# Optimization experiments

Hardware: AMD Instinct MI355X
Metric: run time of the kernel (lower is better)

Reference implementation:

```python
import jax, jax.numpy as jnp
import numpy as np

N = 1024          # sentence length
VW, DW = 100000, 300   # word vocab / embed dim
VP, DP = 64, 100       # pos vocab / embed dim
DV = DW + DP           # len_data_vec = 400 (LSTM in & hidden size)
H = 512                # MLP hidden
F = 128                # feature vec


def _lstm_dir(xs, h0, c0, Wih, Whh, bih, bhh):
    # PyTorch LSTM cell: gates ordered i, f, g, o
    def step(carry, x):
        h, c = carry
        g = x @ Wih.T + bih + h @ Whh.T + bhh
        i, f, gg, o = jnp.split(g, 4)
        i = jax.nn.sigmoid(i)
        f = jax.nn.sigmoid(f)
        gg = jnp.tanh(gg)
        o = jax.nn.sigmoid(o)
        c = f * c + i * gg
        h = o * jnp.tanh(c)
        return (h, c), h
    _, hs = jax.lax.scan(step, (h0, c0), xs)
    return hs  # [n, DV]


def setup_inputs() -> dict:
    key = jax.random.key(0)
    ks = jax.random.split(key, 24)
    s = 0.05
    inp = {
        'word_ids': jax.random.randint(ks[0], (N,), 0, VW),
        'pos_ids': jax.random.randint(ks[1], (N,), 0, VP),
        'h0': jax.random.normal(ks[2], (2, DV), jnp.float32),
        'c0': jax.random.normal(ks[3], (2, DV), jnp.float32),
        'word_emb': jax.random.normal(ks[4], (VW, DW), jnp.float32) * s,
        'pos_emb': jax.random.normal(ks[5], (VP, DP), jnp.float32) * s,
        'Wih_f': jax.random.normal(ks[6], (4 * DV, DV), jnp.float32) * s,
        'Whh_f': jax.random.normal(ks[7], (4 * DV, DV), jnp.float32) * s,
        'bih_f': jax.random.normal(ks[8], (4 * DV,), jnp.float32) * s,
        'bhh_f': jax.random.normal(ks[9], (4 * DV,), jnp.float32) * s,
        'Wih_b': jax.random.normal(ks[10], (4 * DV, DV), jnp.float32) * s,
        'Whh_b': jax.random.normal(ks[11], (4 * DV, DV), jnp.float32) * s,
        'bih_b': jax.random.normal(ks[12], (4 * DV,), jnp.float32) * s,
        'bhh_b': jax.random.normal(ks[13], (4 * DV,), jnp.float32) * s,
        'Wh1': jax.random.normal(ks[14], (H, 2 * DV), jnp.float32) * s,
        'bh1': jax.random.normal(ks[15], (H,), jnp.float32) * s,
        'Wh2': jax.random.normal(ks[16], (F, H), jnp.float32) * s,
        'bh2': jax.random.normal(ks[17], (F,), jnp.float32) * s,
        'Wd1': jax.random.normal(ks[18], (H, 2 * DV), jnp.float32) * s,
        'bd1': jax.random.normal(ks[19], (H,), jnp.float32) * s,
        'Wd2': jax.random.normal(ks[20], (F, H), jnp.float32) * s,
        'bd2': jax.random.normal(ks[21], (F,), jnp.float32) * s,
        'U_1': jax.random.normal(ks[22], (F, F), jnp.float32),
        'u_2': jax.random.normal(ks[23], (1, F), jnp.float32),
    }
    return inp


def reference(word_ids, pos_ids, h0, c0, word_emb, pos_emb,
              Wih_f, Whh_f, bih_f, bhh_f, Wih_b, Whh_b, bih_b, bhh_b,
              Wh1, bh1, Wh2, bh2, Wd1, bd1, Wd2, bd2, U_1, u_2):
    # Embedding gather + concat: x[i] = [word_emb; pos_emb]
    x = jnp.concatenate([word_emb[word_ids], pos_emb[pos_ids]], axis=-1)  # [n, DV]
    # BiLSTM (batch=1): forward dir and reversed dir, concat features
    r_f = _lstm_dir(x, h0[0], c0[0], Wih_f, Whh_f, bih_f, bhh_f)
    r_b = _lstm_dir(x[::-1], h0[1], c0[1], Wih_b, Whh_b, bih_b, bhh_b)[::-1]
    r = jnp.concatenate([r_f, r_b], axis=-1)  # [n, 2*DV]
    sr = jax.nn.sigmoid(r)
    # MLP_head / MLP_dep (clamp(min=0) == relu), batched over all tokens
    Hh = jax.nn.relu(sr @ Wh1.T + bh1) @ Wh2.T + bh2  # [n, F]
    Hd = jax.nn.relu(sr @ Wd1.T + bd1) @ Wd2.T + bd2  # [n, F]
    # Biaffine: adj[i,j] = h_i U h_j^T + h_i u_2^T
    adj = Hh @ U_1 @ Hd.T + Hh @ u_2.T  # [n, n] + [n, 1] broadcast
    return adj
```

## Files before the change

kernel.cpp:

```cpp
#include <hip/hip_runtime.h>
#include <math.h>

#define N_TOK 1024
#define DV    400
#define G4    1600
#define DWD   300
#define DPD   100
#define HID   512
#define FD    128
#define GWG   50
#define EPW   8
#define NCHK  (DV/4)

typedef unsigned uint32x4 __attribute__((ext_vector_type(4)));

__device__ __forceinline__ float sigmoidf_(float x){ return 1.0f/(1.0f+__expf(-x)); }
__device__ __forceinline__ float tanh_safe(float x){
    float t = __expf(-2.0f*fabsf(x));
    float r = (1.0f - t)/(1.0f + t);
    return copysignf(r, x);
}

#define LDA4(p) __hip_atomic_load((p), __ATOMIC_RELAXED, __HIP_MEMORY_SCOPE_AGENT)

#define PLD(X, P) asm volatile("global_load_dwordx4 %0, %1, off sc0 sc1" \
                               : "+&v"(X) : "v"(P) : "memory")
#define PWT(X)    asm volatile("s_waitcnt vmcnt(2)" : "+v"(X) :: "memory")

__global__ void k_gather(const int* __restrict__ wid, const int* __restrict__ pid,
                         const float* __restrict__ wemb, const float* __restrict__ pemb,
                         float* __restrict__ x)
{
    int t = blockIdx.x;
    int w = wid[t], p = pid[t];
    for (int k = threadIdx.x; k < DV; k += blockDim.x){
        float v = (k < DWD) ? wemb[(long)w*DWD + k] : pemb[p*DPD + (k - DWD)];
        x[t*DV + k] = v;
    }
}

__global__ void k_transpose(const float* __restrict__ U, float* __restrict__ Ut, int n)
{
    int j = blockIdx.y*16 + threadIdx.y;
    int k = blockIdx.x*16 + threadIdx.x;
    if (j < n && k < n) Ut[j*n + k] = U[k*n + j];
}

__global__ __launch_bounds__(256) void k_gemm_nt(
    const float* __restrict__ A, const float* __restrict__ B,
    const float* __restrict__ bias1, const float* __restrict__ rowbias,
    float* __restrict__ C, int M, int Nn, int K)
{
    const int BM = 64, BN = 64, BK = 16;
    __shared__ float As[BK][BM];
    __shared__ float Bs[BK][BN];
    int tid = threadIdx.x;
    int tx = tid & 15, ty = tid >> 4;
    int m0 = blockIdx.y*BM, n0 = blockIdx.x*BN;
    int lrow = tid >> 2, lk = (tid & 3) * 4;
    float acc[4][4] = {{0.f}};
    for (int k0 = 0; k0 < K; k0 += BK){
        const float4 av = *(const float4*)&A[(long)(m0+lrow)*K + k0 + lk];
        const float4 bv = *(const float4*)&B[(long)(n0+lrow)*K + k0 + lk];
        As[lk+0][lrow]=av.x; As[lk+1][lrow]=av.y; As[lk+2][lrow]=av.z; As[lk+3][lrow]=av.w;
        Bs[lk+0][lrow]=bv.x; Bs[lk+1][lrow]=bv.y; Bs[lk+2][lrow]=bv.z; Bs[lk+3][lrow]=bv.w;
        __syncthreads();
        #pragma unroll
        for (int kk = 0; kk < BK; ++kk){
            const float4 a = *(const float4*)&As[kk][ty*4];
            const float4 b = *(const float4*)&Bs[kk][tx*4];
            const float ar[4]={a.x,a.y,a.z,a.w}, br[4]={b.x,b.y,b.z,b.w};
            #pragma unroll
            for (int i=0;i<4;++i)
                #pragma unroll
                for (int j=0;j<4;++j) acc[i][j] += ar[i]*br[j];
        }
        __syncthreads();
    }
    #pragma unroll
    for (int i=0;i<4;++i){
        int m = m0 + ty*4 + i;
        float rb = rowbias ? rowbias[m] : 0.0f;
        #pragma unroll
        for (int j=0;j<4;++j){
            int n = n0 + tx*4 + j;
            float v = acc[i][j] + rb;
            if (bias1) v += bias1[n];
            C[(long)m*Nn + n] = v;
        }
    }
}

__global__ __launch_bounds__(256) void k_gemm_ntz(
    const float* __restrict__ A0, const float* __restrict__ A1,
    const float* __restrict__ B0, const float* __restrict__ B1,
    const float* __restrict__ c10, const float* __restrict__ c11,
    const float* __restrict__ c20, const float* __restrict__ c21,
    float* __restrict__ C0, float* __restrict__ C1,
    int M, int Nn, int K, int rev1, int relu)
{
    const float* A = blockIdx.z ? A1 : A0;
    const float* B = blockIdx.z ? B1 : B0;
    const float* bias1 = blockIdx.z ? c11 : c10;
    const float* bias2 = blockIdx.z ? c21 : c20;
    float* C = blockIdx.z ? C1 : C0;
    int revA = blockIdx.z ? rev1 : 0;

    const int BM = 64, BN = 64, BK = 16;
    __shared__ float As[BK][BM];
    __shared__ float Bs[BK][BN];
    int tid = threadIdx.x;
    int tx = tid & 15, ty = tid >> 4;
    int m0 = blockIdx.y*BM, n0 = blockIdx.x*BN;
    int lrow = tid >> 2, lk = (tid & 3) * 4;
    float acc[4][4] = {{0.f}};
    for (int k0 = 0; k0 < K; k0 += BK){
        int am = m0 + lrow; if (revA) am = M - 1 - am;
        const float4 av = *(const float4*)&A[(long)am*K + k0 + lk];
        const float4 bv = *(const float4*)&B[(long)(n0+lrow)*K + k0 + lk];
        As[lk+0][lrow]=av.x; As[lk+1][lrow]=av.y; As[lk+2][lrow]=av.z; As[lk+3][lrow]=av.w;
        Bs[lk+0][lrow]=bv.x; Bs[lk+1][lrow]=bv.y; Bs[lk+2][lrow]=bv.z; Bs[lk+3][lrow]=bv.w;
        __syncthreads();
        #pragma unroll
        for (int kk = 0; kk < BK; ++kk){
            const float4 a = *(const float4*)&As[kk][ty*4];
            const float4 b = *(const float4*)&Bs[kk][tx*4];
            const float ar[4]={a.x,a.y,a.z,a.w}, br[4]={b.x,b.y,b.z,b.w};
            #pragma unroll
            for (int i=0;i<4;++i)
                #pragma unroll
                for (int j=0;j<4;++j) acc[i][j] += ar[i]*br[j];
        }
        __syncthreads();
    }
    #pragma unroll
    for (int i=0;i<4;++i){
        int m = m0 + ty*4 + i;
        #pragma unroll
        for (int j=0;j<4;++j){
            int n = n0 + tx*4 + j;
            float v = acc[i][j];
            if (bias1) v += bias1[n];
            if (bias2) v += bias2[n];
            if (relu)  v = fmaxf(v, 0.0f);
            C[(long)m*Nn + n] = v;
        }
    }
}

__global__ __launch_bounds__(256) void k_lstm(
    const float* __restrict__ Whh_f, const float* __restrict__ Whh_b,
    const float* __restrict__ Xf, const float* __restrict__ Xb,
    const float* __restrict__ h0, const float* __restrict__ c0,
    unsigned* __restrict__ mbox)
{
    __shared__ float W_s[32][DV];
    __shared__ __align__(16) float hA[DV];
    __shared__ __align__(16) float hB[DV];

    int tid = threadIdx.x;
    int dir = blockIdx.x / GWG;
    int g   = blockIdx.x % GWG;
    int j0  = g * EPW;
    const float* Whh = dir ? Whh_b : Whh_f;
    const float* XX  = dir ? Xb    : Xf;
    unsigned* mb = mbox + (size_t)dir * N_TOK * DV;

    for (int idx = tid; idx < 32*DV; idx += 256){
        int rr = idx / DV, k = idx % DV;
        int grow_ = (rr >> 3) * DV + j0 + (rr & 7);
        W_s[rr][k] = Whh[(long)grow_*DV + k];
    }
    for (int idx = tid; idx < DV; idx += 256) hA[idx] = h0[dir*DV + idx];

    int w    = tid >> 6;
    int lane = tid & 63;
    int q    = lane >> 4;
    int eo   = (lane >> 3) & 1;
    int l    = lane & 7;
    int e    = 2*w + eo;
    int r    = q*8 + e;
    int grow = q*DV + j0 + e;
    bool owner = (q == 0) && (l == 0);
    float c_reg = owner ? c0[dir*DV + j0 + e] : 0.0f;

    int  cid   = tid;
    bool isPoll = (tid < NCHK) && (cid != 2*g) && (cid != 2*g + 1);
    __syncthreads();

    float xv_n = (l == 0) ? XX[grow] : 0.0f;

    bool dead = false;
    for (int t = 0; t < N_TOK; ++t){
        const float* hc = (t & 1) ? hB : hA;
        float*       hn = (t & 1) ? hA : hB;

        const unsigned* pc = mb + (size_t)t*DV + 4*cid;
        uint32x4 A = {0,0,0,0}, B = {0,0,0,0}, C = {0,0,0,0};
        if (isPoll){ PLD(A, pc); PLD(B, pc); PLD(C, pc); }

        float xv = xv_n;

        const float2* wrow = (const float2*)&W_s[r][0];
        const float2* hp   = (const float2*)hc;
        float sum = 0.0f;
        #pragma unroll
        for (int i = 0; i < 25; ++i){
            float2 wv = wrow[l + 8*i];
            float2 hv = hp[l + 8*i];
            sum = fmaf(wv.x, hv.x, sum);
            sum = fmaf(wv.y, hv.y, sum);
        }
        sum += __shfl_xor(sum, 1, 8);
        sum += __shfl_xor(sum, 2, 8);
        sum += __shfl_xor(sum, 4, 8);
        if (l == 0) sum += xv;

        float gi = __shfl(sum, eo*8 + 0,  64);
        float gf = __shfl(sum, eo*8 + 16, 64);
        float gg = __shfl(sum, eo*8 + 32, 64);
        float go = __shfl(sum, eo*8 + 48, 64);

        if (owner){
            float iv = sigmoidf_(gi), fv = sigmoidf_(gf);
            float gv = tanh_safe(gg), ov = sigmoidf_(go);
            c_reg = fv*c_reg + iv*gv;
            float hvv = ov * tanh_safe(c_reg);
            unsigned pk = __float_as_uint(hvv) | 1u;
            __hip_atomic_store(mb + (size_t)t*DV + j0 + e, pk,
                               __ATOMIC_RELAXED, __HIP_MEMORY_SCOPE_AGENT);
            hn[j0 + e] = hvv;
        }

        if (l == 0){
            int tn = (t + 1 < N_TOK) ? (t + 1) : t;
            xv_n = XX[(size_t)tn*G4 + grow];
        }

        if (isPoll && !dead){
            bool got = false;
            uint32x4 R;
            int fast = 0;
            while (fast < 64){
                PWT(A); if (A.x && A.y && A.z && A.w){ R = A; got = true; break; }
                PLD(A, pc);
                PWT(B); if (B.x && B.y && B.z && B.w){ R = B; got = true; break; }
                PLD(B, pc);
                PWT(C); if (C.x && C.y && C.z && C.w){ R = C; got = true; break; }
                PLD(C, pc);
                fast += 3;
            }
            if (got){
                float4 f;
                f.x = __uint_as_float(R.x); f.y = __uint_as_float(R.y);
                f.z = __uint_as_float(R.z); f.w = __uint_as_float(R.w);
                *(float4*)&hn[4*cid] = f;
            } else {
                bool d0=false,d1=false,d2=false,d3=false;
                int guard = 0;
                while (!(d0 && d1 && d2 && d3)){
                    if (!d0){ unsigned u = LDA4(pc+0); if (u){ hn[4*cid+0]=__uint_as_float(u); d0=true; } }
                    if (!d1){ unsigned u = LDA4(pc+1); if (u){ hn[4*cid+1]=__uint_as_float(u); d1=true; } }
                    if (!d2){ unsigned u = LDA4(pc+2); if (u){ hn[4*cid+2]=__uint_as_float(u); d2=true; } }
                    if (!d3){ unsigned u = LDA4(pc+3); if (u){ hn[4*cid+3]=__uint_as_float(u); d3=true; } }
                    if (++guard > (1 << 18)) { dead = true; break; }
                }
            }
        }
        __syncthreads();
    }
}

__global__ void k_sr(const float* __restrict__ mbox, float* __restrict__ sr)
{
    int t = blockIdx.x;
    const float* mF = mbox;
    const float* mB = mbox + (size_t)N_TOK * DV;
    for (int c = threadIdx.x; c < 2*DV; c += blockDim.x){
        float v = (c < DV) ? mF[(size_t)t*DV + c]
                           : mB[(size_t)(N_TOK-1-t)*DV + (c - DV)];
        sr[t*2*DV + c] = 1.0f/(1.0f+__expf(-v));
    }
}

__global__ void k_bvec(const float* __restrict__ Hh, const float* __restrict__ u2,
                       float* __restrict__ bvec)
{
    int i = blockIdx.x;
    int lane = threadIdx.x;
    float v = Hh[i*FD + lane]*u2[lane] + Hh[i*FD + 64 + lane]*u2[64 + lane];
    v += __shfl_xor(v, 1, 64);
    v += __shfl_xor(v, 2, 64);
    v += __shfl_xor(v, 4, 64);
    v += __shfl_xor(v, 8, 64);
    v += __shfl_xor(v, 16, 64);
    v += __shfl_xor(v, 32, 64);
    if (lane == 0) bvec[i] = v;
}

extern "C" void kernel_launch(void* const* d_in, const int* in_sizes, int n_in,
                              void* d_out, int out_size, void* d_ws, size_t ws_size,
                              hipStream_t stream)
{
    const int*   word_ids = (const int*)  d_in[0];
    const int*   pos_ids  = (const int*)  d_in[1];
    const float* h0    = (const float*)d_in[2];
    const float* c0    = (const float*)d_in[3];
    const float* wemb  = (const float*)d_in[4];
    const float* pemb  = (const float*)d_in[5];
    const float* Wih_f = (const float*)d_in[6];
    const float* Whh_f = (const float*)d_in[7];
    const float* bih_f = (const float*)d_in[8];
    const float* bhh_f = (const float*)d_in[9];
    const float* Wih_b = (const float*)d_in[10];
    const float* Whh_b = (const float*)d_in[11];
    const float* bih_b = (const float*)d_in[12];
    const float* bhh_b = (const float*)d_in[13];
    const float* Wh1   = (const float*)d_in[14];
    const float* bh1   = (const float*)d_in[15];
    const float* Wh2   = (const float*)d_in[16];
    const float* bh2   = (const float*)d_in[17];
    const float* Wd1   = (const float*)d_in[18];
    const float* bd1   = (const float*)d_in[19];
    const float* Wd2   = (const float*)d_in[20];
    const float* bd2   = (const float*)d_in[21];
    const float* U1    = (const float*)d_in[22];
    const float* u2    = (const float*)d_in[23];
    float* out = (float*)d_out;

    float* ws  = (float*)d_ws;
    float* x    = ws;
    float* Xf   = ws + 409600;
    float* Xb   = ws + 2048000;
    unsigned* mbox = (unsigned*)(ws + 3686400);
    float* sr   = ws + 4505600;
    float* T1h  = ws + 5324800;
    float* T1d  = ws + 5849088;
    float* Hh   = ws + 6373376;
    float* Hd   = ws + 6504448;
    float* G1   = ws + 6635520;
    float* Ut   = ws + 6766592;
    float* bvec = ws + 6782976;

    hipMemsetAsync(mbox, 0, (size_t)2*N_TOK*DV*sizeof(unsigned), stream);

    k_gather<<<N_TOK, 128, 0, stream>>>(word_ids, pos_ids, wemb, pemb, x);
    k_transpose<<<dim3(8,8), dim3(16,16), 0, stream>>>(U1, Ut, FD);

    dim3 blk(256);
    k_gemm_ntz<<<dim3(G4/64, N_TOK/64, 2), blk, 0, stream>>>(
        x, x, Wih_f, Wih_b, bih_f, bih_b, bhh_f, bhh_b, Xf, Xb,
        N_TOK, G4, DV, 1, 0);

    k_lstm<<<2*GWG, 256, 0, stream>>>(Whh_f, Whh_b, Xf, Xb, h0, c0, mbox);

    k_sr<<<N_TOK, 256, 0, stream>>>((const float*)mbox, sr);

    k_gemm_ntz<<<dim3(HID/64, N_TOK/64, 2), blk, 0, stream>>>(
        sr, sr, Wh1, Wd1, bh1, bd1, nullptr, nullptr, T1h, T1d,
        N_TOK, HID, 2*DV, 0, 1);
    k_gemm_ntz<<<dim3(FD/64, N_TOK/64, 2), blk, 0, stream>>>(
        T1h, T1d, Wh2, Wd2, bh2, bd2, nullptr, nullptr, Hh, Hd,
        N_TOK, FD, HID, 0, 0);
    k_bvec<<<N_TOK, 64, 0, stream>>>(Hh, u2, bvec);
    k_gemm_nt<<<dim3(FD/64,  N_TOK/64), blk, 0, stream>>>(Hh, Ut, nullptr, nullptr, G1,
                                                          N_TOK, FD, FD);
    k_gemm_nt<<<dim3(N_TOK/64, N_TOK/64), blk, 0, stream>>>(G1, Hd, nullptr, bvec, out,
                                                            N_TOK, N_TOK, FD);
}
```

Measured before the change: 2.926 ms.

## Pin each LSTM direction to one XCC and poll XCC-local L2 mailbox

Launches many blocks and keeps only those on XCC 0 and 1, assigning each direction's 50 workgroups through an atomic ticket so every block of a direction shares one L2. The h-exchange then writes a fast mailbox with sc0 stores and polls it with sc0 loads, which stay coherent within the XCC instead of going to device scope. A shadow copy is still written with agent-scope atomics and serves as a fallback after repeated fast-poll timeouts, and k_sr reads from it. The scheme assumes enough co-resident blocks land on each XCC, and it adds a second mailbox plus launch overhead for the blocks that exit immediately.

```diff
diff --git a/kernel.cpp b/kernel.cpp
--- a/kernel.cpp
+++ b/kernel.cpp
@@ -23,9 +23,9 @@
 
 #define LDA4(p) __hip_atomic_load((p), __ATOMIC_RELAXED, __HIP_MEMORY_SCOPE_AGENT)
 
-#define PLD(X, P) asm volatile("global_load_dwordx4 %0, %1, off sc0 sc1" \
-                               : "+&v"(X) : "v"(P) : "memory")
-#define PWT(X)    asm volatile("s_waitcnt vmcnt(2)" : "+v"(X) :: "memory")
+#define PLDF(X, P) asm volatile("global_load_dwordx4 %0, %1, off sc0" \
+                                : "+&v"(X) : "v"(P) : "memory")
+#define WT0(X)     asm volatile("s_waitcnt vmcnt(0)" : "+v"(X) :: "memory")
 
 __global__ void k_gather(const int* __restrict__ wid, const int* __restrict__ pid,
                          const float* __restrict__ wemb, const float* __restrict__ pemb,
@@ -152,19 +152,30 @@
     const float* __restrict__ Whh_f, const float* __restrict__ Whh_b,
     const float* __restrict__ Xf, const float* __restrict__ Xb,
     const float* __restrict__ h0, const float* __restrict__ c0,
-    unsigned* __restrict__ mbox)
+    unsigned* __restrict__ fastm, unsigned* __restrict__ shadow,
+    int* __restrict__ tickets)
 {
     __shared__ float W_s[32][DV];
     __shared__ __align__(16) float hA[DV];
     __shared__ __align__(16) float hB[DV];
+    __shared__ int rank_s;
+
+    unsigned xcc;
+    asm volatile("s_getreg_b32 %0, hwreg(HW_REG_XCC_ID)" : "=s"(xcc));
+    if (xcc > 1) return;
 
     int tid = threadIdx.x;
-    int dir = blockIdx.x / GWG;
-    int g   = blockIdx.x % GWG;
+    int dir = (int)xcc;
+    if (tid == 0) rank_s = atomicAdd(&tickets[dir], 1);
+    __syncthreads();
+    int g = rank_s;
+    if (g >= GWG) return;
+
     int j0  = g * EPW;
     const float* Whh = dir ? Whh_b : Whh_f;
     const float* XX  = dir ? Xb    : Xf;
-    unsigned* mb = mbox + (size_t)dir * N_TOK * DV;
+    unsigned* fm = fastm  + (size_t)dir * N_TOK * DV;
+    unsigned* sh = shadow + (size_t)dir * N_TOK * DV;
 
     for (int idx = tid; idx < 32*DV; idx += 256){
         int rr = idx / DV, k = idx % DV;
@@ -184,21 +195,17 @@
     bool owner = (q == 0) && (l == 0);
     float c_reg = owner ? c0[dir*DV + j0 + e] : 0.0f;
 
-    int  cid   = tid;
+    int  cid    = tid;
     bool isPoll = (tid < NCHK) && (cid != 2*g) && (cid != 2*g + 1);
     __syncthreads();
 
     float xv_n = (l == 0) ? XX[grow] : 0.0f;
 
-    bool dead = false;
+    bool dead = false, useFast = true;
+    int  fastFails = 0;
     for (int t = 0; t < N_TOK; ++t){
         const float* hc = (t & 1) ? hB : hA;
         float*       hn = (t & 1) ? hA : hB;
-
-        const unsigned* pc = mb + (size_t)t*DV + 4*cid;
-        uint32x4 A = {0,0,0,0}, B = {0,0,0,0}, C = {0,0,0,0};
-        if (isPoll){ PLD(A, pc); PLD(B, pc); PLD(C, pc); }
-
         float xv = xv_n;
 
         const float2* wrow = (const float2*)&W_s[r][0];
@@ -227,7 +234,10 @@
             c_reg = fv*c_reg + iv*gv;
             float hvv = ov * tanh_safe(c_reg);
             unsigned pk = __float_as_uint(hvv) | 1u;
-            __hip_atomic_store(mb + (size_t)t*DV + j0 + e, pk,
+            unsigned* fs = fm + (size_t)t*DV + j0 + e;
+            asm volatile("global_store_dword %0, %1, off sc0"
+                         :: "v"(fs), "v"(pk) : "memory");
+            __hip_atomic_store(sh + (size_t)t*DV + j0 + e, pk,
                                __ATOMIC_RELAXED, __HIP_MEMORY_SCOPE_AGENT);
             hn[j0 + e] = hvv;
         }
@@ -238,31 +248,36 @@
         }
 
         if (isPoll && !dead){
+            const unsigned* pf = fm + (size_t)t*DV + 4*cid;
+            const unsigned* ps = sh + (size_t)t*DV + 4*cid;
             bool got = false;
-            uint32x4 R;
-            int fast = 0;
-            while (fast < 64){
-                PWT(A); if (A.x && A.y && A.z && A.w){ R = A; got = true; break; }
-                PLD(A, pc);
-                PWT(B); if (B.x && B.y && B.z && B.w){ R = B; got = true; break; }
-                PLD(B, pc);
-                PWT(C); if (C.x && C.y && C.z && C.w){ R = C; got = true; break; }
-                PLD(C, pc);
-                fast += 3;
+            if (useFast){
+                uint32x4 A = {0,0,0,0};
+                PLDF(A, pf);
+                int it = 0;
+                for (;;){
+                    WT0(A);
+                    if (A.x && A.y && A.z && A.w){ got = true; break; }
+                    if (++it > 32) break;
+                    PLDF(A, pf);
+                }
+                if (got){
+                    float4 f;
+                    f.x = __uint_as_float(A.x); f.y = __uint_as_float(A.y);
+                    f.z = __uint_as_float(A.z); f.w = __uint_as_float(A.w);
+                    *(float4*)&hn[4*cid] = f;
+                } else {
+                    if (++fastFails >= 2) useFast = false;
+                }
             }
-            if (got){
-                float4 f;
-                f.x = __uint_as_float(R.x); f.y = __uint_as_float(R.y);
-                f.z = __uint_as_float(R.z); f.w = __uint_as_float(R.w);
-                *(float4*)&hn[4*cid] = f;
-            } else {
+            if (!got){
                 bool d0=false,d1=false,d2=false,d3=false;
                 int guard = 0;
                 while (!(d0 && d1 && d2 && d3)){
-                    if (!d0){ unsigned u = LDA4(pc+0); if (u){ hn[4*cid+0]=__uint_as_float(u); d0=true; } }
-                    if (!d1){ unsigned u = LDA4(pc+1); if (u){ hn[4*cid+1]=__uint_as_float(u); d1=true; } }
-                    if (!d2){ unsigned u = LDA4(pc+2); if (u){ hn[4*cid+2]=__uint_as_float(u); d2=true; } }
-                    if (!d3){ unsigned u = LDA4(pc+3); if (u){ hn[4*cid+3]=__uint_as_float(u); d3=true; } }
+                    if (!d0){ unsigned u = LDA4(ps+0); if (u){ hn[4*cid+0]=__uint_as_float(u); d0=true; } }
+                    if (!d1){ unsigned u = LDA4(ps+1); if (u){ hn[4*cid+1]=__uint_as_float(u); d1=true; } }
+                    if (!d2){ unsigned u = LDA4(ps+2); if (u){ hn[4*cid+2]=__uint_as_float(u); d2=true; } }
+                    if (!d3){ unsigned u = LDA4(ps+3); if (u){ hn[4*cid+3]=__uint_as_float(u); d3=true; } }
                     if (++guard > (1 << 18)) { dead = true; break; }
                 }
             }
@@ -271,11 +286,11 @@
     }
 }
 
-__global__ void k_sr(const float* __restrict__ mbox, float* __restrict__ sr)
+__global__ void k_sr(const float* __restrict__ shadow, float* __restrict__ sr)
 {
     int t = blockIdx.x;
-    const float* mF = mbox;
-    const float* mB = mbox + (size_t)N_TOK * DV;
+    const float* mF = shadow;
+    const float* mB = shadow + (size_t)N_TOK * DV;
     for (int c = threadIdx.x; c < 2*DV; c += blockDim.x){
         float v = (c < DV) ? mF[(size_t)t*DV + c]
                            : mB[(size_t)(N_TOK-1-t)*DV + (c - DV)];
@@ -332,17 +347,20 @@
     float* x    = ws;
     float* Xf   = ws + 409600;
     float* Xb   = ws + 2048000;
-    unsigned* mbox = (unsigned*)(ws + 3686400);
-    float* sr   = ws + 4505600;
-    float* T1h  = ws + 5324800;
-    float* T1d  = ws + 5849088;
-    float* Hh   = ws + 6373376;
-    float* Hd   = ws + 6504448;
-    float* G1   = ws + 6635520;
-    float* Ut   = ws + 6766592;
-    float* bvec = ws + 6782976;
-
-    hipMemsetAsync(mbox, 0, (size_t)2*N_TOK*DV*sizeof(unsigned), stream);
+    unsigned* fastm  = (unsigned*)(ws + 3686400);
+    unsigned* shadow = (unsigned*)(ws + 4505600);
+    float* sr   = ws + 5324800;
+    float* T1h  = ws + 6144000;
+    float* T1d  = ws + 6668288;
+    float* Hh   = ws + 7192576;
+    float* Hd   = ws + 7323648;
+    float* G1   = ws + 7454720;
+    float* Ut   = ws + 7585792;
+    float* bvec = ws + 7602176;
+    int*   tickets = (int*)(ws + 7603200);
+
+    hipMemsetAsync(fastm, 0, (size_t)2 * 2*N_TOK*DV*sizeof(unsigned), stream);
+    hipMemsetAsync(tickets, 0, 2*sizeof(int), stream);
 
     k_gather<<<N_TOK, 128, 0, stream>>>(word_ids, pos_ids, wemb, pemb, x);
     k_transpose<<<dim3(8,8), dim3(16,16), 0, stream>>>(U1, Ut, FD);
@@ -352,9 +370,10 @@
         x, x, Wih_f, Wih_b, bih_f, bih_b, bhh_f, bhh_b, Xf, Xb,
         N_TOK, G4, DV, 1, 0);
 
-    k_lstm<<<2*GWG, 256, 0, stream>>>(Whh_f, Whh_b, Xf, Xb, h0, c0, mbox);
-
-    k_sr<<<N_TOK, 256, 0, stream>>>((const float*)mbox, sr);
+    k_lstm<<<2048, 256, 0, stream>>>(Whh_f, Whh_b, Xf, Xb, h0, c0,
+                                     fastm, shadow, tickets);
+
+    k_sr<<<N_TOK, 256, 0, stream>>>((const float*)shadow, sr);
 
     k_gemm_ntz<<<dim3(HID/64, N_TOK/64, 2), blk, 0, stream>>>(
         sr, sr, Wh1, Wd1, bh1, bd1, nullptr, nullptr, T1h, T1d,
```

New measurement: 4.294 ms. 1.47x slower.

## Pad LSTM mailbox slots and poll per-element with scalar atomic loads

Applied to the files above, without the earlier changes.

The cross-block h-exchange mailbox is padded so each hidden element sits in its own 16-byte slot. Each thread now polls two scalar elements with a three-deep pipeline of relaxed atomic loads, replacing the earlier dwordx4 chunk polling done through inline asm. The next-step X prefetch is moved earlier, and workspace buffers are reshuffled so the larger mailbox fits. The aim is to avoid waiting on whole 4-element chunks and to reduce false sharing in the per-step handoff, at the cost of four times the mailbox memory and more load instructions per step.

```diff
diff --git a/kernel.cpp b/kernel.cpp
--- a/kernel.cpp
+++ b/kernel.cpp
@@ -10,9 +10,7 @@
 #define FD    128
 #define GWG   50
 #define EPW   8
-#define NCHK  (DV/4)
-
-typedef unsigned uint32x4 __attribute__((ext_vector_type(4)));
+#define PAD   4
 
 __device__ __forceinline__ float sigmoidf_(float x){ return 1.0f/(1.0f+__expf(-x)); }
 __device__ __forceinline__ float tanh_safe(float x){
@@ -21,11 +19,7 @@
     return copysignf(r, x);
 }
 
-#define LDA4(p) __hip_atomic_load((p), __ATOMIC_RELAXED, __HIP_MEMORY_SCOPE_AGENT)
-
-#define PLD(X, P) asm volatile("global_load_dwordx4 %0, %1, off sc0 sc1" \
-                               : "+&v"(X) : "v"(P) : "memory")
-#define PWT(X)    asm volatile("s_waitcnt vmcnt(2)" : "+v"(X) :: "memory")
+#define LDA(p) __hip_atomic_load((p), __ATOMIC_RELAXED, __HIP_MEMORY_SCOPE_AGENT)
 
 __global__ void k_gather(const int* __restrict__ wid, const int* __restrict__ pid,
                          const float* __restrict__ wemb, const float* __restrict__ pemb,
@@ -164,7 +158,7 @@
     int j0  = g * EPW;
     const float* Whh = dir ? Whh_b : Whh_f;
     const float* XX  = dir ? Xb    : Xf;
-    unsigned* mb = mbox + (size_t)dir * N_TOK * DV;
+    unsigned* mb = mbox + (size_t)dir * N_TOK * DV * PAD;
 
     for (int idx = tid; idx < 32*DV; idx += 256){
         int rr = idx / DV, k = idx % DV;
@@ -184,8 +178,9 @@
     bool owner = (q == 0) && (l == 0);
     float c_reg = owner ? c0[dir*DV + j0 + e] : 0.0f;
 
-    int  cid   = tid;
-    bool isPoll = (tid < NCHK) && (cid != 2*g) && (cid != 2*g + 1);
+    int s0 = tid, s1 = 256 + tid;
+    bool own0  = (s0 >= j0) && (s0 < j0 + EPW);
+    bool skip1 = (tid >= DV - 256) || ((s1 >= j0) && (s1 < j0 + EPW));
     __syncthreads();
 
     float xv_n = (l == 0) ? XX[grow] : 0.0f;
@@ -195,11 +190,19 @@
         const float* hc = (t & 1) ? hB : hA;
         float*       hn = (t & 1) ? hA : hB;
 
-        const unsigned* pc = mb + (size_t)t*DV + 4*cid;
-        uint32x4 A = {0,0,0,0}, B = {0,0,0,0}, C = {0,0,0,0};
-        if (isPoll){ PLD(A, pc); PLD(B, pc); PLD(C, pc); }
+        unsigned* rowb = mb + (size_t)t*DV*PAD;
+        const unsigned* p0 = rowb + (size_t)s0*PAD;
+        const unsigned* p1 = rowb + (size_t)((tid < DV-256) ? s1 : s0)*PAD;
+
+        unsigned q0a = LDA(p0), q1a = LDA(p1);
+        unsigned q0b = LDA(p0), q1b = LDA(p1);
+        unsigned q0c = LDA(p0), q1c = LDA(p1);
 
         float xv = xv_n;
+        if (l == 0){
+            int tn = (t + 1 < N_TOK) ? (t + 1) : t;
+            xv_n = XX[(size_t)tn*G4 + grow];
+        }
 
         const float2* wrow = (const float2*)&W_s[r][0];
         const float2* hp   = (const float2*)hc;
@@ -227,58 +230,40 @@
             c_reg = fv*c_reg + iv*gv;
             float hvv = ov * tanh_safe(c_reg);
             unsigned pk = __float_as_uint(hvv) | 1u;
-            __hip_atomic_store(mb + (size_t)t*DV + j0 + e, pk,
+            __hip_atomic_store(rowb + (size_t)(j0 + e)*PAD, pk,
                                __ATOMIC_RELAXED, __HIP_MEMORY_SCOPE_AGENT);
             hn[j0 + e] = hvv;
         }
 
-        if (l == 0){
-            int tn = (t + 1 < N_TOK) ? (t + 1) : t;
-            xv_n = XX[(size_t)tn*G4 + grow];
-        }
-
-        if (isPoll && !dead){
-            bool got = false;
-            uint32x4 R;
-            int fast = 0;
-            while (fast < 64){
-                PWT(A); if (A.x && A.y && A.z && A.w){ R = A; got = true; break; }
-                PLD(A, pc);
-                PWT(B); if (B.x && B.y && B.z && B.w){ R = B; got = true; break; }
-                PLD(B, pc);
-                PWT(C); if (C.x && C.y && C.z && C.w){ R = C; got = true; break; }
-                PLD(C, pc);
-                fast += 3;
+        if (!dead){
+            bool g0 = own0, g1 = skip1;
+            int guard = 0;
+            while (!(g0 && g1)){
+                if (!g0){
+                    if (q0a){ hn[s0] = __uint_as_float(q0a); g0 = true; }
+                    else { q0a = q0b; q0b = q0c; q0c = LDA(p0); }
+                }
+                if (!g1){
+                    if (q1a){ hn[s1] = __uint_as_float(q1a); g1 = true; }
+                    else { q1a = q1b; q1b = q1c; q1c = LDA(p1); }
+                }
+                if (++guard > (1 << 18)) { dead = true; break; }
             }
-            if (got){
-                float4 f;
-                f.x = __uint_as_float(R.x); f.y = __uint_as_float(R.y);
-                f.z = __uint_as_float(R.z); f.w = __uint_as_float(R.w);
-                *(float4*)&hn[4*cid] = f;
-            } else {
-                bool d0=false,d1=false,d2=false,d3=false;
-                int guard = 0;
-                while (!(d0 && d1 && d2 && d3)){
-                    if (!d0){ unsigned u = LDA4(pc+0); if (u){ hn[4*cid+0]=__uint_as_float(u); d0=true; } }
-                    if (!d1){ unsigned u = LDA4(pc+1); if (u){ hn[4*cid+1]=__uint_as_float(u); d1=true; } }
-                    if (!d2){ unsigned u = LDA4(pc+2); if (u){ hn[4*cid+2]=__uint_as_float(u); d2=true; } }
-                    if (!d3){ unsigned u = LDA4(pc+3); if (u){ hn[4*cid+3]=__uint_as_float(u); d3=true; } }
-                    if (++guard > (1 << 18)) { dead = true; break; }
-                }
-            }
-        }
-        __syncthreads();
-    }
-}
-
-__global__ void k_sr(const float* __restrict__ mbox, float* __restrict__ sr)
+        }
+        __syncthreads();
+    }
+}
+
+__global__ void k_sr(const unsigned* __restrict__ mbox, float* __restrict__ sr)
 {
     int t = blockIdx.x;
-    const float* mF = mbox;
-    const float* mB = mbox + (size_t)N_TOK * DV;
+    const unsigned* mF = mbox;
+    const unsigned* mB = mbox + (size_t)N_TOK * DV * PAD;
     for (int c = threadIdx.x; c < 2*DV; c += blockDim.x){
-        float v = (c < DV) ? mF[(size_t)t*DV + c]
-                           : mB[(size_t)(N_TOK-1-t)*DV + (c - DV)];
+        unsigned u = (c < DV)
+            ? LDA(mF + ((size_t)t*DV + c)*PAD)
+            : LDA(mB + ((size_t)(N_TOK-1-t)*DV + (c - DV))*PAD);
+        float v = __uint_as_float(u);
         sr[t*2*DV + c] = 1.0f/(1.0f+__expf(-v));
     }
 }
@@ -333,16 +318,16 @@
     float* Xf   = ws + 409600;
     float* Xb   = ws + 2048000;
     unsigned* mbox = (unsigned*)(ws + 3686400);
-    float* sr   = ws + 4505600;
-    float* T1h  = ws + 5324800;
-    float* T1d  = ws + 5849088;
-    float* Hh   = ws + 6373376;
-    float* Hd   = ws + 6504448;
-    float* G1   = ws + 6635520;
-    float* Ut   = ws + 6766592;
-    float* bvec = ws + 6782976;
-
-    hipMemsetAsync(mbox, 0, (size_t)2*N_TOK*DV*sizeof(unsigned), stream);
+    float* Ut   = ws + 6963200;
+    float* bvec = ws + 6979584;
+    float* sr   = ws + 409600;
+    float* T1h  = ws + 1228800;
+    float* T1d  = ws + 1753088;
+    float* Hh   = ws + 2277376;
+    float* Hd   = ws + 2408448;
+    float* G1   = ws + 2539520;
+
+    hipMemsetAsync(mbox, 0, (size_t)2*N_TOK*DV*PAD*sizeof(unsigned), stream);
 
     k_gather<<<N_TOK, 128, 0, stream>>>(word_ids, pos_ids, wemb, pemb, x);
     k_transpose<<<dim3(8,8), dim3(16,16), 0, stream>>>(U1, Ut, FD);
@@ -354,7 +339,7 @@
 
     k_lstm<<<2*GWG, 256, 0, stream>>>(Whh_f, Whh_b, Xf, Xb, h0, c0, mbox);
 
-    k_sr<<<N_TOK, 256, 0, stream>>>((const float*)mbox, sr);
+    k_sr<<<N_TOK, 256, 0, stream>>>(mbox, sr);
 
     k_gemm_ntz<<<dim3(HID/64, N_TOK/64, 2), blk, 0, stream>>>(
         sr, sr, Wh1, Wd1, bh1, bd1, nullptr, nullptr, T1h, T1d,
```

After: 3.193 ms. 9.1% more time.
